# Kernel tuning notes

Hardware: AMD Instinct MI355X
Metric: run time of the kernel (lower is better)

The kernel has to match this reference:

```python
import jax, jax.numpy as jnp
import numpy as np


def setup_inputs() -> dict:
    key = jax.random.key(0)
    k1, k2, k3, k4 = jax.random.split(key, 4)
    d_in, d_out, B, T = 1024, 1024, 4, 2048
    scale = 1.0 / np.sqrt(d_in)
    return {
        "x": jax.random.normal(k1, (B, T, d_in), dtype=jnp.float32),
        "Wq": jax.random.normal(k2, (d_in, d_out), dtype=jnp.float32) * scale,
        "Wk": jax.random.normal(k3, (d_in, d_out), dtype=jnp.float32) * scale,
        "Wv": jax.random.normal(k4, (d_in, d_out), dtype=jnp.float32) * scale,
    }


def reference(x, Wq, Wk, Wv):
    # x: [B, T, d_in]; Wq/Wk/Wv: [d_in, d_out] (Linear, bias=False)
    q = jnp.einsum("btd,de->bte", x, Wq)
    k = jnp.einsum("btd,de->bte", x, Wk)
    v = jnp.einsum("btd,de->bte", x, Wv)
    d_out = k.shape[-1]
    scores = jnp.einsum("bqe,bke->bqk", q, k)  # [B, T, T]
    T = x.shape[1]
    causal = jnp.triu(jnp.ones((T, T), dtype=bool), k=1)  # True above diagonal
    scores = jnp.where(causal[None, :, :], -jnp.inf, scores)
    # original divides after masking; -inf stays -inf so math is identical
    att = jax.nn.softmax(scores / jnp.sqrt(jnp.asarray(d_out, scores.dtype)), axis=-1)
    # dropout p=0.0 -> identity
    return jnp.einsum("bqk,bke->bqe", att, v)
```

## Files before the change

kernel.cpp:

```cpp
#include <hip/hip_runtime.h>
#include <stdint.h>
#include <math.h>

typedef unsigned short u16;
typedef __bf16 bf16x8 __attribute__((ext_vector_type(8)));
typedef float f32x4 __attribute__((ext_vector_type(4)));

#define BM 128
#define BN 128
#define BK 32

enum { M_QKV = 0, M_SCORE = 1, M_PV = 2 };

__device__ __forceinline__ u16 f2bf(float f) {
    union { float f; unsigned int u; } a; a.f = f;
    unsigned int u = a.u;
    u += 0x7FFFu + ((u >> 16) & 1u);
    return (u16)(u >> 16);
}

__device__ __forceinline__ void async_load16(const void* g, void* l) {
    __builtin_amdgcn_global_load_lds(
        (const __attribute__((address_space(1))) void*)g,
        (__attribute__((address_space(3))) void*)l,
        16, 0, 0);
}

template<int MODE>
__global__ __launch_bounds__(256)
void gemm_bt(const u16* __restrict__ A, long long sAb,
             const u16* __restrict__ Bt, long long sBb,
             void* __restrict__ Cv, long long sCb,
             float* __restrict__ rowsum,
             int M, int N, int K, float kfac)
{
    int bm, bn;
    if (MODE == M_SCORE) {
        const int idx = blockIdx.x;
        bm = (int)((sqrtf(8.f * idx + 1.f) - 1.f) * 0.5f);
        while ((bm + 1) * (bm + 2) / 2 <= idx) ++bm;
        while (bm * (bm + 1) / 2 > idx) --bm;
        bn = idx - bm * (bm + 1) / 2;
    } else {
        bn = blockIdx.x; bm = blockIdx.y;
    }
    const int bz = blockIdx.z;
    A  += (size_t)bz * sAb;
    Bt += (size_t)bz * sBb;

    const int tid  = threadIdx.x;
    const int lane = tid & 63;
    const int wv   = tid >> 6;
    const int wm   = wv >> 1;
    const int wn   = wv & 1;

    __shared__ __attribute__((aligned(16))) u16 As[BM * BK];
    __shared__ __attribute__((aligned(16))) u16 Bs[BN * BK];

    f32x4 acc[4][4] = {};

    const int rowA0 = bm * BM, rowB0 = bn * BN;
    const int srow = lane >> 2;
    const int scol = (((lane & 3) ^ ((lane >> 3) & 3)) * 8);

    int kEnd = K;
    if (MODE == M_PV) { int ke = (bm + 1) * BM; kEnd = ke < K ? ke : K; }

    const int lm   = lane & 15;
    const int quad = lane >> 4;
    const int lk   = (quad ^ ((lm >> 1) & 3)) * 8;

    for (int k0 = 0; k0 < kEnd; k0 += BK) {
        #pragma unroll
        for (int c = 0; c < 2; ++c) {
            const int cc = wv * 2 + c;
            const int r  = cc * 16 + srow;
            async_load16(&A [(size_t)(rowA0 + r) * K + k0 + scol], &As[cc * 512 + lane * 8]);
            async_load16(&Bt[(size_t)(rowB0 + r) * K + k0 + scol], &Bs[cc * 512 + lane * 8]);
        }
        __syncthreads();

        bf16x8 af[4], bfr[4];
        #pragma unroll
        for (int i = 0; i < 4; ++i)
            af[i] = *reinterpret_cast<const bf16x8*>(&As[(wm * 64 + i * 16 + lm) * BK + lk]);
        #pragma unroll
        for (int j = 0; j < 4; ++j)
            bfr[j] = *reinterpret_cast<const bf16x8*>(&Bs[(wn * 64 + j * 16 + lm) * BK + lk]);
        #pragma unroll
        for (int i = 0; i < 4; ++i)
            #pragma unroll
            for (int j = 0; j < 4; ++j)
                acc[i][j] = __builtin_amdgcn_mfma_f32_16x16x32_bf16(af[i], bfr[j], acc[i][j], 0, 0, 0);
        __syncthreads();
    }

    if (MODE == M_QKV) {
        u16* C = (u16*)Cv + (size_t)(bn >> 3) * sCb;
        #pragma unroll
        for (int i = 0; i < 4; ++i)
            #pragma unroll
            for (int j = 0; j < 4; ++j) {
                const int r0 = rowA0 + wm * 64 + i * 16 + quad * 4;
                const int c0 = (rowB0 + wn * 64 + j * 16 + lm) & 1023;
                #pragma unroll
                for (int g = 0; g < 4; ++g)
                    C[(size_t)(r0 + g) * 1024 + c0] = f2bf(acc[i][j][g]);
            }
    } else if (MODE == M_SCORE) {
        u16* E = (u16*)Cv + (size_t)bz * sCb;
        float rs[4][4];
        #pragma unroll
        for (int i = 0; i < 4; ++i)
            #pragma unroll
            for (int g = 0; g < 4; ++g) rs[i][g] = 0.f;
        #pragma unroll
        for (int i = 0; i < 4; ++i)
            #pragma unroll
            for (int j = 0; j < 4; ++j) {
                const int r0 = rowA0 + wm * 64 + i * 16 + quad * 4;
                const int c  = rowB0 + wn * 64 + j * 16 + lm;
                #pragma unroll
                for (int g = 0; g < 4; ++g) {
                    const int r = r0 + g;
                    float e = (c <= r) ? exp2f(acc[i][j][g] * kfac) : 0.f;
                    E[(size_t)r * N + c] = f2bf(e);
                    rs[i][g] += e;
                }
            }
        #pragma unroll
        for (int i = 0; i < 4; ++i)
            #pragma unroll
            for (int g = 0; g < 4; ++g) {
                float v = rs[i][g];
                v += __shfl_xor(v, 1); v += __shfl_xor(v, 2);
                v += __shfl_xor(v, 4); v += __shfl_xor(v, 8);
                rs[i][g] = v;
            }
        if (lm == 0) {
            #pragma unroll
            for (int i = 0; i < 4; ++i)
                #pragma unroll
                for (int g = 0; g < 4; ++g) {
                    const int r = rowA0 + wm * 64 + i * 16 + quad * 4 + g;
                    atomicAdd(&rowsum[(size_t)bz * M + r], rs[i][g]);
                }
        }
    } else {
        float* C = (float*)Cv + (size_t)bz * sCb;
        #pragma unroll
        for (int i = 0; i < 4; ++i) {
            const int r0 = rowA0 + wm * 64 + i * 16 + quad * 4;
            float inv[4];
            #pragma unroll
            for (int g = 0; g < 4; ++g)
                inv[g] = 1.f / rowsum[(size_t)bz * M + r0 + g];
            #pragma unroll
            for (int j = 0; j < 4; ++j) {
                const int c0 = rowB0 + wn * 64 + j * 16 + lm;
                #pragma unroll
                for (int g = 0; g < 4; ++g)
                    C[(size_t)(r0 + g) * N + c0] = acc[i][j][g] * inv[g];
            }
        }
    }
}

__global__ __launch_bounds__(256)
void cast_x(const float* __restrict__ x, u16* __restrict__ o, long long n)
{
    long long i = ((long long)blockIdx.x * blockDim.x + threadIdx.x) * 8;
    if (i >= n) return;
    const float4 a = *(const float4*)(x + i);
    const float4 b = *(const float4*)(x + i + 4);
    union { u16 u[8]; float4 v; } r;
    r.u[0] = f2bf(a.x); r.u[1] = f2bf(a.y); r.u[2] = f2bf(a.z); r.u[3] = f2bf(a.w);
    r.u[4] = f2bf(b.x); r.u[5] = f2bf(b.y); r.u[6] = f2bf(b.z); r.u[7] = f2bf(b.w);
    *(float4*)(o + i) = r.v;
}

__global__ __launch_bounds__(256)
void castT_w(const float* __restrict__ W, u16* __restrict__ Wt, int rows, int cols)
{
    __shared__ u16 t[32][33];
    const int c0 = blockIdx.x * 32, r0 = blockIdx.y * 32;
    const int tx = threadIdx.x & 31, ty = threadIdx.x >> 5;
    #pragma unroll
    for (int s = 0; s < 32; s += 8)
        t[ty + s][tx] = f2bf(W[(size_t)(r0 + ty + s) * cols + c0 + tx]);
    __syncthreads();
    #pragma unroll
    for (int s = 0; s < 32; s += 8)
        Wt[(size_t)(c0 + ty + s) * rows + r0 + tx] = t[tx][ty + s];
}

__global__ __launch_bounds__(256)
void transpose_b(const u16* __restrict__ V, long long sVb,
                 u16* __restrict__ Vt, long long sVtb, int rows, int cols)
{
    V  += (size_t)blockIdx.z * sVb;
    Vt += (size_t)blockIdx.z * sVtb;
    __shared__ u16 t[32][33];
    const int c0 = blockIdx.x * 32, r0 = blockIdx.y * 32;
    const int tx = threadIdx.x & 31, ty = threadIdx.x >> 5;
    #pragma unroll
    for (int s = 0; s < 32; s += 8)
        t[ty + s][tx] = V[(size_t)(r0 + ty + s) * cols + c0 + tx];
    __syncthreads();
    #pragma unroll
    for (int s = 0; s < 32; s += 8)
        Vt[(size_t)(c0 + ty + s) * rows + r0 + tx] = t[tx][ty + s];
}

extern "C" void kernel_launch(void* const* d_in, const int* in_sizes, int n_in,
                              void* d_out, int out_size, void* d_ws, size_t ws_size,
                              hipStream_t stream)
{
    const int B = 4, T = 2048, D = 1024;
    const float* x  = (const float*)d_in[0];
    const float* Wq = (const float*)d_in[1];
    const float* Wk = (const float*)d_in[2];
    const float* Wv = (const float*)d_in[3];
    float* out = (float*)d_out;

    const size_t nX = (size_t)B * T * D;
    u16* Xb = (u16*)d_ws;
    u16* Wt = Xb + nX;
    u16* Q  = Wt + 3 * (size_t)D * D;
    u16* Kb = Q + nX;
    u16* Vb = Kb + nX;
    char* rest = (char*)(Vb + nX);
    const size_t fixed   = (size_t)((char*)rest - (char*)d_ws);
    const size_t perb_E  = (size_t)T * T * 2;
    const size_t perb_Vt = (size_t)D * T * 2;
    const size_t perb_rs = (size_t)T * 4;
    const bool full = ws_size >= fixed + (size_t)B * (perb_E + perb_Vt + perb_rs);
    const int nb = full ? B : 1;
    u16*   E  = (u16*)rest;
    u16*   Vt = E + nb * (size_t)T * T;
    float* RS = (float*)(Vt + nb * (size_t)D * T);

    const float kfac = 1.4426950408889634f / 32.0f;
    const int nTri = (T / BM) * (T / BM + 1) / 2;

    cast_x<<<dim3((unsigned)(nX / (8 * 256))), 256, 0, stream>>>(x, Xb, (long long)nX);
    castT_w<<<dim3(D / 32, D / 32), 256, 0, stream>>>(Wq, Wt,                     D, D);
    castT_w<<<dim3(D / 32, D / 32), 256, 0, stream>>>(Wk, Wt + (size_t)D * D,     D, D);
    castT_w<<<dim3(D / 32, D / 32), 256, 0, stream>>>(Wv, Wt + 2 * (size_t)D * D, D, D);

    gemm_bt<M_QKV><<<dim3(3 * D / BN, (B * T) / BM, 1), 256, 0, stream>>>(
        Xb, 0, Wt, 0, Q, (long long)nX, nullptr, B * T, 3 * D, D, 0.f);

    if (full) {
        hipMemsetAsync(RS, 0, (size_t)B * T * 4, stream);
        gemm_bt<M_SCORE><<<dim3(nTri, 1, B), 256, 0, stream>>>(
            Q, (long long)T * D, Kb, (long long)T * D, E, (long long)T * T, RS, T, T, D, kfac);
        transpose_b<<<dim3(D / 32, T / 32, B), 256, 0, stream>>>(
            Vb, (long long)T * D, Vt, (long long)D * T, T, D);
        gemm_bt<M_PV><<<dim3(D / BN, T / BM, B), 256, 0, stream>>>(
            E, (long long)T * T, Vt, (long long)D * T, out, (long long)T * D, RS, T, D, T, 0.f);
    } else {
        for (int b = 0; b < B; ++b) {
            const size_t ob = (size_t)b * T * D;
            hipMemsetAsync(RS, 0, (size_t)T * 4, stream);
            gemm_bt<M_SCORE><<<dim3(nTri, 1, 1), 256, 0, stream>>>(
                Q + ob, 0, Kb + ob, 0, E, 0, RS, T, T, D, kfac);
            transpose_b<<<dim3(D / 32, T / 32, 1), 256, 0, stream>>>(Vb + ob, 0, Vt, 0, T, D);
            gemm_bt<M_PV><<<dim3(D / BN, T / BM, 1), 256, 0, stream>>>(
                E, 0, Vt, 0, out + ob, 0, RS, T, D, T, 0.f);
        }
    }
}
```

Measured before the change: 275.5 us.

## Fuse V transpose into QKV GEMM epilogue and use 64x128 attention tiles

The QKV projection epilogue now writes V directly in transposed [B, D, T] layout using packed 4-element stores, so the separate transpose kernel and the intermediate V buffer are gone. The three weight cast/transpose launches are merged into one 3D-grid launch. The score and PV GEMMs switch to 64x128 tiles with a new triangular index mapping, giving finer causal granularity and more blocks. The risks are lower per-block data reuse with the smaller M tile and strided transposed stores in the QKV epilogue.

```diff
diff --git a/kernel.cpp b/kernel.cpp
--- a/kernel.cpp
+++ b/kernel.cpp
@@ -6,8 +6,6 @@
 typedef __bf16 bf16x8 __attribute__((ext_vector_type(8)));
 typedef float f32x4 __attribute__((ext_vector_type(4)));
 
-#define BM 128
-#define BN 128
 #define BK 32
 
 enum { M_QKV = 0, M_SCORE = 1, M_PV = 2 };
@@ -26,21 +24,25 @@
         16, 0, 0);
 }
 
-template<int MODE>
+template<int MODE, int TBM, int TBN>
 __global__ __launch_bounds__(256)
 void gemm_bt(const u16* __restrict__ A, long long sAb,
              const u16* __restrict__ Bt, long long sBb,
              void* __restrict__ Cv, long long sCb,
-             float* __restrict__ rowsum,
+             float* __restrict__ rowsum, u16* __restrict__ vt,
              int M, int N, int K, float kfac)
 {
+    constexpr int NI  = TBM / 32, NJ  = TBN / 32;
+    constexpr int ACH = TBM / 64, BCH = TBN / 64;
+
     int bm, bn;
     if (MODE == M_SCORE) {
         const int idx = blockIdx.x;
-        bm = (int)((sqrtf(8.f * idx + 1.f) - 1.f) * 0.5f);
-        while ((bm + 1) * (bm + 2) / 2 <= idx) ++bm;
-        while (bm * (bm + 1) / 2 > idx) --bm;
-        bn = idx - bm * (bm + 1) / 2;
+        int w = (int)sqrtf((float)idx + 0.5f);
+        while (w * w > idx) --w;
+        while ((w + 1) * (w + 1) <= idx) ++w;
+        if (idx < w * w + w) { bm = 2 * w - 1; bn = idx - w * w; }
+        else                 { bm = 2 * w;     bn = idx - (w * w + w); }
     } else {
         bn = blockIdx.x; bm = blockIdx.y;
     }
@@ -54,17 +56,17 @@
     const int wm   = wv >> 1;
     const int wn   = wv & 1;
 
-    __shared__ __attribute__((aligned(16))) u16 As[BM * BK];
-    __shared__ __attribute__((aligned(16))) u16 Bs[BN * BK];
-
-    f32x4 acc[4][4] = {};
-
-    const int rowA0 = bm * BM, rowB0 = bn * BN;
+    __shared__ __attribute__((aligned(16))) u16 As[TBM * BK];
+    __shared__ __attribute__((aligned(16))) u16 Bs[TBN * BK];
+
+    f32x4 acc[NI][NJ] = {};
+
+    const int rowA0 = bm * TBM, rowB0 = bn * TBN;
     const int srow = lane >> 2;
     const int scol = (((lane & 3) ^ ((lane >> 3) & 3)) * 8);
 
     int kEnd = K;
-    if (MODE == M_PV) { int ke = (bm + 1) * BM; kEnd = ke < K ? ke : K; }
+    if (MODE == M_PV) { int ke = (bm + 1) * TBM; kEnd = ke < K ? ke : K; }
 
     const int lm   = lane & 15;
     const int quad = lane >> 4;
@@ -72,54 +74,75 @@
 
     for (int k0 = 0; k0 < kEnd; k0 += BK) {
         #pragma unroll
-        for (int c = 0; c < 2; ++c) {
-            const int cc = wv * 2 + c;
+        for (int c = 0; c < ACH; ++c) {
+            const int cc = wv * ACH + c;
             const int r  = cc * 16 + srow;
-            async_load16(&A [(size_t)(rowA0 + r) * K + k0 + scol], &As[cc * 512 + lane * 8]);
+            async_load16(&A[(size_t)(rowA0 + r) * K + k0 + scol], &As[cc * 512 + lane * 8]);
+        }
+        #pragma unroll
+        for (int c = 0; c < BCH; ++c) {
+            const int cc = wv * BCH + c;
+            const int r  = cc * 16 + srow;
             async_load16(&Bt[(size_t)(rowB0 + r) * K + k0 + scol], &Bs[cc * 512 + lane * 8]);
         }
         __syncthreads();
 
-        bf16x8 af[4], bfr[4];
-        #pragma unroll
-        for (int i = 0; i < 4; ++i)
-            af[i] = *reinterpret_cast<const bf16x8*>(&As[(wm * 64 + i * 16 + lm) * BK + lk]);
-        #pragma unroll
-        for (int j = 0; j < 4; ++j)
-            bfr[j] = *reinterpret_cast<const bf16x8*>(&Bs[(wn * 64 + j * 16 + lm) * BK + lk]);
-        #pragma unroll
-        for (int i = 0; i < 4; ++i)
-            #pragma unroll
-            for (int j = 0; j < 4; ++j)
+        bf16x8 af[NI], bfr[NJ];
+        #pragma unroll
+        for (int i = 0; i < NI; ++i)
+            af[i] = *reinterpret_cast<const bf16x8*>(&As[(wm * (TBM / 2) + i * 16 + lm) * BK + lk]);
+        #pragma unroll
+        for (int j = 0; j < NJ; ++j)
+            bfr[j] = *reinterpret_cast<const bf16x8*>(&Bs[(wn * (TBN / 2) + j * 16 + lm) * BK + lk]);
+        #pragma unroll
+        for (int i = 0; i < NI; ++i)
+            #pragma unroll
+            for (int j = 0; j < NJ; ++j)
                 acc[i][j] = __builtin_amdgcn_mfma_f32_16x16x32_bf16(af[i], bfr[j], acc[i][j], 0, 0, 0);
         __syncthreads();
     }
 
     if (MODE == M_QKV) {
-        u16* C = (u16*)Cv + (size_t)(bn >> 3) * sCb;
-        #pragma unroll
-        for (int i = 0; i < 4; ++i)
-            #pragma unroll
-            for (int j = 0; j < 4; ++j) {
-                const int r0 = rowA0 + wm * 64 + i * 16 + quad * 4;
-                const int c0 = (rowB0 + wn * 64 + j * 16 + lm) & 1023;
-                #pragma unroll
-                for (int g = 0; g < 4; ++g)
-                    C[(size_t)(r0 + g) * 1024 + c0] = f2bf(acc[i][j][g]);
-            }
+        if (bn < 16) {
+            u16* C = (u16*)Cv + (size_t)(bn >> 3) * sCb;
+            #pragma unroll
+            for (int i = 0; i < NI; ++i)
+                #pragma unroll
+                for (int j = 0; j < NJ; ++j) {
+                    const int r0 = rowA0 + wm * (TBM / 2) + i * 16 + quad * 4;
+                    const int c0 = (rowB0 + wn * (TBN / 2) + j * 16 + lm) & 1023;
+                    #pragma unroll
+                    for (int g = 0; g < 4; ++g)
+                        C[(size_t)(r0 + g) * 1024 + c0] = f2bf(acc[i][j][g]);
+                }
+        } else {
+            #pragma unroll
+            for (int i = 0; i < NI; ++i) {
+                const int r0 = rowA0 + wm * (TBM / 2) + i * 16 + quad * 4;
+                const int b  = r0 >> 11, t0 = r0 & 2047;
+                #pragma unroll
+                for (int j = 0; j < NJ; ++j) {
+                    const int c0 = (rowB0 + wn * (TBN / 2) + j * 16 + lm) & 1023;
+                    ushort4 pk;
+                    pk.x = f2bf(acc[i][j][0]); pk.y = f2bf(acc[i][j][1]);
+                    pk.z = f2bf(acc[i][j][2]); pk.w = f2bf(acc[i][j][3]);
+                    *(ushort4*)&vt[((size_t)b << 21) + ((size_t)c0 << 11) + t0] = pk;
+                }
+            }
+        }
     } else if (MODE == M_SCORE) {
         u16* E = (u16*)Cv + (size_t)bz * sCb;
-        float rs[4][4];
-        #pragma unroll
-        for (int i = 0; i < 4; ++i)
+        float rs[NI][4];
+        #pragma unroll
+        for (int i = 0; i < NI; ++i)
             #pragma unroll
             for (int g = 0; g < 4; ++g) rs[i][g] = 0.f;
         #pragma unroll
-        for (int i = 0; i < 4; ++i)
-            #pragma unroll
-            for (int j = 0; j < 4; ++j) {
-                const int r0 = rowA0 + wm * 64 + i * 16 + quad * 4;
-                const int c  = rowB0 + wn * 64 + j * 16 + lm;
+        for (int i = 0; i < NI; ++i)
+            #pragma unroll
+            for (int j = 0; j < NJ; ++j) {
+                const int r0 = rowA0 + wm * (TBM / 2) + i * 16 + quad * 4;
+                const int c  = rowB0 + wn * (TBN / 2) + j * 16 + lm;
                 #pragma unroll
                 for (int g = 0; g < 4; ++g) {
                     const int r = r0 + g;
@@ -129,7 +152,7 @@
                 }
             }
         #pragma unroll
-        for (int i = 0; i < 4; ++i)
+        for (int i = 0; i < NI; ++i)
             #pragma unroll
             for (int g = 0; g < 4; ++g) {
                 float v = rs[i][g];
@@ -139,25 +162,25 @@
             }
         if (lm == 0) {
             #pragma unroll
-            for (int i = 0; i < 4; ++i)
+            for (int i = 0; i < NI; ++i)
                 #pragma unroll
                 for (int g = 0; g < 4; ++g) {
-                    const int r = rowA0 + wm * 64 + i * 16 + quad * 4 + g;
+                    const int r = rowA0 + wm * (TBM / 2) + i * 16 + quad * 4 + g;
                     atomicAdd(&rowsum[(size_t)bz * M + r], rs[i][g]);
                 }
         }
     } else {
         float* C = (float*)Cv + (size_t)bz * sCb;
         #pragma unroll
-        for (int i = 0; i < 4; ++i) {
-            const int r0 = rowA0 + wm * 64 + i * 16 + quad * 4;
+        for (int i = 0; i < NI; ++i) {
+            const int r0 = rowA0 + wm * (TBM / 2) + i * 16 + quad * 4;
             float inv[4];
             #pragma unroll
             for (int g = 0; g < 4; ++g)
                 inv[g] = 1.f / rowsum[(size_t)bz * M + r0 + g];
             #pragma unroll
-            for (int j = 0; j < 4; ++j) {
-                const int c0 = rowB0 + wn * 64 + j * 16 + lm;
+            for (int j = 0; j < NJ; ++j) {
+                const int c0 = rowB0 + wn * (TBN / 2) + j * 16 + lm;
                 #pragma unroll
                 for (int g = 0; g < 4; ++g)
                     C[(size_t)(r0 + g) * N + c0] = acc[i][j][g] * inv[g];
@@ -180,36 +203,21 @@
 }
 
 __global__ __launch_bounds__(256)
-void castT_w(const float* __restrict__ W, u16* __restrict__ Wt, int rows, int cols)
-{
+void castT_w3(const float* __restrict__ W0, const float* __restrict__ W1,
+              const float* __restrict__ W2, u16* __restrict__ Wt, int D)
+{
+    const float* W = blockIdx.z == 0 ? W0 : (blockIdx.z == 1 ? W1 : W2);
+    u16* dst = Wt + (size_t)blockIdx.z * D * D;
     __shared__ u16 t[32][33];
     const int c0 = blockIdx.x * 32, r0 = blockIdx.y * 32;
     const int tx = threadIdx.x & 31, ty = threadIdx.x >> 5;
     #pragma unroll
     for (int s = 0; s < 32; s += 8)
-        t[ty + s][tx] = f2bf(W[(size_t)(r0 + ty + s) * cols + c0 + tx]);
+        t[ty + s][tx] = f2bf(W[(size_t)(r0 + ty + s) * D + c0 + tx]);
     __syncthreads();
     #pragma unroll
     for (int s = 0; s < 32; s += 8)
-        Wt[(size_t)(c0 + ty + s) * rows + r0 + tx] = t[tx][ty + s];
-}
-
-__global__ __launch_bounds__(256)
-void transpose_b(const u16* __restrict__ V, long long sVb,
-                 u16* __restrict__ Vt, long long sVtb, int rows, int cols)
-{
-    V  += (size_t)blockIdx.z * sVb;
-    Vt += (size_t)blockIdx.z * sVtb;
-    __shared__ u16 t[32][33];
-    const int c0 = blockIdx.x * 32, r0 = blockIdx.y * 32;
-    const int tx = threadIdx.x & 31, ty = threadIdx.x >> 5;
-    #pragma unroll
-    for (int s = 0; s < 32; s += 8)
-        t[ty + s][tx] = V[(size_t)(r0 + ty + s) * cols + c0 + tx];
-    __syncthreads();
-    #pragma unroll
-    for (int s = 0; s < 32; s += 8)
-        Vt[(size_t)(c0 + ty + s) * rows + r0 + tx] = t[tx][ty + s];
+        dst[(size_t)(c0 + ty + s) * D + r0 + tx] = t[tx][ty + s];
 }
 
 extern "C" void kernel_launch(void* const* d_in, const int* in_sizes, int n_in,
@@ -228,46 +236,41 @@
     u16* Wt = Xb + nX;
     u16* Q  = Wt + 3 * (size_t)D * D;
     u16* Kb = Q + nX;
-    u16* Vb = Kb + nX;
-    char* rest = (char*)(Vb + nX);
-    const size_t fixed   = (size_t)((char*)rest - (char*)d_ws);
-    const size_t perb_E  = (size_t)T * T * 2;
-    const size_t perb_Vt = (size_t)D * T * 2;
+    u16* Vt = Kb + nX;
+    char* rest = (char*)(Vt + nX);
+    const size_t fixed  = (size_t)((char*)rest - (char*)d_ws);
+    const size_t perb_E = (size_t)T * T * 2;
     const size_t perb_rs = (size_t)T * 4;
-    const bool full = ws_size >= fixed + (size_t)B * (perb_E + perb_Vt + perb_rs);
+    const bool full = ws_size >= fixed + (size_t)B * (perb_E + perb_rs);
     const int nb = full ? B : 1;
     u16*   E  = (u16*)rest;
-    u16*   Vt = E + nb * (size_t)T * T;
-    float* RS = (float*)(Vt + nb * (size_t)D * T);
+    float* RS = (float*)(E + nb * (size_t)T * T);
 
     const float kfac = 1.4426950408889634f / 32.0f;
-    const int nTri = (T / BM) * (T / BM + 1) / 2;
+    const int nTri64 = 272;
 
     cast_x<<<dim3((unsigned)(nX / (8 * 256))), 256, 0, stream>>>(x, Xb, (long long)nX);
-    castT_w<<<dim3(D / 32, D / 32), 256, 0, stream>>>(Wq, Wt,                     D, D);
-    castT_w<<<dim3(D / 32, D / 32), 256, 0, stream>>>(Wk, Wt + (size_t)D * D,     D, D);
-    castT_w<<<dim3(D / 32, D / 32), 256, 0, stream>>>(Wv, Wt + 2 * (size_t)D * D, D, D);
-
-    gemm_bt<M_QKV><<<dim3(3 * D / BN, (B * T) / BM, 1), 256, 0, stream>>>(
-        Xb, 0, Wt, 0, Q, (long long)nX, nullptr, B * T, 3 * D, D, 0.f);
+    castT_w3<<<dim3(D / 32, D / 32, 3), 256, 0, stream>>>(Wq, Wk, Wv, Wt, D);
+
+    gemm_bt<M_QKV, 128, 128><<<dim3(3 * D / 128, (B * T) / 128, 1), 256, 0, stream>>>(
+        Xb, 0, Wt, 0, Q, (long long)nX, nullptr, Vt, B * T, 3 * D, D, 0.f);
 
     if (full) {
         hipMemsetAsync(RS, 0, (size_t)B * T * 4, stream);
-        gemm_bt<M_SCORE><<<dim3(nTri, 1, B), 256, 0, stream>>>(
-            Q, (long long)T * D, Kb, (long long)T * D, E, (long long)T * T, RS, T, T, D, kfac);
-        transpose_b<<<dim3(D / 32, T / 32, B), 256, 0, stream>>>(
-            Vb, (long long)T * D, Vt, (long long)D * T, T, D);
-        gemm_bt<M_PV><<<dim3(D / BN, T / BM, B), 256, 0, stream>>>(
-            E, (long long)T * T, Vt, (long long)D * T, out, (long long)T * D, RS, T, D, T, 0.f);
+        gemm_bt<M_SCORE, 64, 128><<<dim3(nTri64, 1, B), 256, 0, stream>>>(
+            Q, (long long)T * D, Kb, (long long)T * D, E, (long long)T * T, RS, nullptr,
+            T, T, D, kfac);
+        gemm_bt<M_PV, 64, 128><<<dim3(D / 128, T / 64, B), 256, 0, stream>>>(
+            E, (long long)T * T, Vt, (long long)D * T, out, (long long)T * D, RS, nullptr,
+            T, D, T, 0.f);
     } else {
         for (int b = 0; b < B; ++b) {
             const size_t ob = (size_t)b * T * D;
             hipMemsetAsync(RS, 0, (size_t)T * 4, stream);
-            gemm_bt<M_SCORE><<<dim3(nTri, 1, 1), 256, 0, stream>>>(
-                Q + ob, 0, Kb + ob, 0, E, 0, RS, T, T, D, kfac);
-            transpose_b<<<dim3(D / 32, T / 32, 1), 256, 0, stream>>>(Vb + ob, 0, Vt, 0, T, D);
-            gemm_bt<M_PV><<<dim3(D / BN, T / BM, 1), 256, 0, stream>>>(
-                E, 0, Vt, 0, out + ob, 0, RS, T, D, T, 0.f);
-        }
-    }
-}
+            gemm_bt<M_SCORE, 64, 128><<<dim3(nTri64, 1, 1), 256, 0, stream>>>(
+                Q + ob, 0, Kb + ob, 0, E, 0, RS, nullptr, T, T, D, kfac);
+            gemm_bt<M_PV, 64, 128><<<dim3(D / 128, T / 64, 1), 256, 0, stream>>>(
+                E, 0, Vt + (size_t)b * D * T, 0, out + ob, 0, RS, nullptr, T, D, T, 0.f);
+        }
+    }
+}
```

New measurement: 267.2 us. 1.03x faster.
